# Performance work log

Measured on AMD Instinct MI355X. Metric: run time of the kernel, lower is better.

Reference implementation:

```python
import jax, jax.numpy as jnp
import numpy as np

N_NODES = 50000
N_EDGES = 800000
N_GRAPHS = 128
D_IN, D_HID, D_OUT = 128, 128, 128  # gnn_input_dim, gnn_hidden_dim, gnn_output_dim
EPS = 1e-5
NEG_SLOPE = 0.01


def setup_inputs() -> dict:
    key = jax.random.key(0)
    ks = jax.random.split(key, 16)
    x = jax.random.normal(ks[0], (N_NODES, D_IN), jnp.float32)
    edge_index = jax.random.randint(ks[1], (2, N_EDGES), 0, N_NODES, dtype=jnp.int64)
    batch = jnp.sort(jax.random.randint(ks[2], (N_NODES,), 0, N_GRAPHS, dtype=jnp.int64))

    def lin(k, fi, fo):
        return jax.random.normal(k, (fi, fo), jnp.float32) * (1.0 / np.sqrt(fi))

    d2, d4 = 2 * D_HID, 4 * D_HID
    return {
        "x": x, "edge_index": edge_index, "batch": batch, "batch_size": N_GRAPHS,
        "W1": lin(ks[3], D_IN, d2), "b1": jnp.zeros((d2,), jnp.float32),
        "g1": jnp.ones((d2,), jnp.float32), "be1": jnp.zeros((d2,), jnp.float32),
        "W2": lin(ks[4], d2, d4), "b2": jnp.zeros((d4,), jnp.float32),
        "g2": jnp.ones((d4,), jnp.float32), "be2": jnp.zeros((d4,), jnp.float32),
        "W3": lin(ks[5], d4, d4), "b3": jnp.zeros((d4,), jnp.float32),
        "g3": jnp.ones((d4,), jnp.float32), "be3": jnp.zeros((d4,), jnp.float32),
        "Wf": lin(ks[6], d4, D_OUT), "bf": jnp.zeros((D_OUT,), jnp.float32),
    }


def _layernorm(h, g, b):
    mu = jnp.mean(h, axis=-1, keepdims=True)
    var = jnp.mean(jnp.square(h - mu), axis=-1, keepdims=True)
    return (h - mu) * jax.lax.rsqrt(var + EPS) * g + b


def _gcn_conv(h, W, b, src, dst, norm, n):
    # h' = D^-1/2 (A+I) D^-1/2 (h W) + b   (PyG GCNConv with self-loops)
    m = h @ W                                    # [N, F_out]
    msg = m[src] * norm[:, None]                 # [E+N, F_out]
    return jax.ops.segment_sum(msg, dst, num_segments=n) + b


def reference(x, edge_index, batch, batch_size, W1, b1, g1, be1,
              W2, b2, g2, be2, W3, b3, g3, be3, Wf, bf):
    n = x.shape[0]
    loop = jnp.arange(n, dtype=edge_index.dtype)
    src = jnp.concatenate([edge_index[0], loop])
    dst = jnp.concatenate([edge_index[1], loop])
    deg = jax.ops.segment_sum(jnp.ones_like(dst, dtype=x.dtype), dst, num_segments=n)
    dinv = jax.lax.rsqrt(deg)                    # deg >= 1 due to self loops
    norm = dinv[src] * dinv[dst]

    h = _gcn_conv(x, W1, b1, src, dst, norm, n)
    h = jax.nn.leaky_relu(_layernorm(h, g1, be1), NEG_SLOPE)
    h = _gcn_conv(h, W2, b2, src, dst, norm, n)
    h = jax.nn.leaky_relu(_layernorm(h, g2, be2), NEG_SLOPE)
    h = _gcn_conv(h, W3, b3, src, dst, norm, n)
    h = _layernorm(h, g3, be3)

    # global average pool per graph
    sums = jax.ops.segment_sum(h, batch, num_segments=batch_size)
    cnt = jax.ops.segment_sum(jnp.ones((n,), h.dtype), batch, num_segments=batch_size)
    pooled = sums / jnp.maximum(cnt, 1.0)[:, None]
    return pooled @ Wf + bf
```

## Files before the change

kernel.cpp:

```cpp
#include <hip/hip_runtime.h>
#include <hip/hip_bf16.h>
#include <math.h>

#define GRAPHS 128
#define SCAN_B 256
#define BM 128
#define BN 128
#define PCH 128
#define WSCALE 2097152.0f

typedef __attribute__((ext_vector_type(4))) int i32x4;

__device__ inline unsigned short f2b(float f) {
    unsigned int u = __float_as_uint(f);
    unsigned int r = (u + 0x7fffu + ((u >> 16) & 1u)) >> 16;
    return (unsigned short)r;
}
__device__ inline float b2f(unsigned short u) {
    return __uint_as_float(((unsigned int)u) << 16);
}
__device__ inline void unpack8(float* v, uint4 u) {
    v[0] = b2f(u.x & 0xffffu); v[1] = b2f(u.x >> 16);
    v[2] = b2f(u.y & 0xffffu); v[3] = b2f(u.y >> 16);
    v[4] = b2f(u.z & 0xffffu); v[5] = b2f(u.z >> 16);
    v[6] = b2f(u.w & 0xffffu); v[7] = b2f(u.w >> 16);
}

__device__ inline void gload16(const void* g, void* l) {
    typedef unsigned int __attribute__((address_space(1))) gu32;
    typedef unsigned int __attribute__((address_space(3))) su32;
    __builtin_amdgcn_global_load_lds((const gu32*)g, (su32*)l, 16, 0, 0);
}

__device__ inline int xcd_vid(int p, int nwg) {
    int q = nwg >> 3, r = nwg & 7, x = p & 7, ix = p >> 3;
    return (x < r ? x * (q + 1) : r * (q + 1) + (x - r) * q) + ix;
}


__global__ void k_count(const int* __restrict__ dst, int* __restrict__ cnt, int E) {
    int i = blockIdx.x * blockDim.x + threadIdx.x;
    if (i < E) atomicAdd(&cnt[dst[i]], 1);
}

__global__ void k_scan1(const int* __restrict__ cnt, int* __restrict__ excl,
                        int* __restrict__ bsum, int n) {
    __shared__ int sh[SCAN_B];
    int t = threadIdx.x;
    int i = blockIdx.x * SCAN_B + t;
    int v = (i < n) ? cnt[i] : 0;
    sh[t] = v;
    __syncthreads();
    for (int off = 1; off < SCAN_B; off <<= 1) {
        int x = (t >= off) ? sh[t - off] : 0;
        __syncthreads();
        sh[t] += x;
        __syncthreads();
    }
    if (i < n) excl[i] = sh[t] - v;
    if (t == SCAN_B - 1) bsum[blockIdx.x] = sh[t];
}

__global__ void k_scan2(int* __restrict__ bsum, int nb) {
    __shared__ int sh[SCAN_B];
    int t = threadIdx.x;
    int v = (t < nb) ? bsum[t] : 0;
    sh[t] = v;
    __syncthreads();
    for (int off = 1; off < SCAN_B; off <<= 1) {
        int x = (t >= off) ? sh[t - off] : 0;
        __syncthreads();
        sh[t] += x;
        __syncthreads();
    }
    if (t < nb) bsum[t] = sh[t] - v;
}

__global__ void k_scan3(int* __restrict__ rowstart, const int* __restrict__ bsum,
                        const int* __restrict__ cnt, float* __restrict__ dinv,
                        int* __restrict__ cursor, int n, int E) {
    int i = blockIdx.x * SCAN_B + threadIdx.x;
    if (i < n) {
        rowstart[i] += bsum[blockIdx.x];
        cursor[i] = 0;
        dinv[i] = rsqrtf((float)cnt[i] + 1.0f);
    }
    if (i == 0) rowstart[n] = E;
}

__global__ void k_scatter_csr(const int* __restrict__ src, const int* __restrict__ dst,
                              const float* __restrict__ dinv, const int* __restrict__ rowstart,
                              int* __restrict__ cursor, int2* __restrict__ csr, int E) {
    int e = blockIdx.x * blockDim.x + threadIdx.x;
    if (e >= E) return;
    int s = src[e], d = dst[e];
    int pos = rowstart[d] + atomicAdd(&cursor[d], 1);
    int2 c;
    c.x = s;
    c.y = __float_as_int(dinv[s] * dinv[d]);
    csr[pos] = c;
}


__global__ void k_prep(const float* __restrict__ W1, const float* __restrict__ W2,
                       const float* __restrict__ W3, signed char* __restrict__ T1,
                       signed char* __restrict__ T2, signed char* __restrict__ T3,
                       float* __restrict__ S1, float* __restrict__ S2,
                       float* __restrict__ S3, const float* __restrict__ x,
                       signed char* __restrict__ qx, float* __restrict__ sx,
                       int n, int mpad) {
    int lane = threadIdx.x & 63;
    if (blockIdx.x < 320) {
        int w = blockIdx.x * 4 + (threadIdx.x >> 6);
        const float* W; signed char* T; float* S; int K, N, col;
        if (w < 256) { W = W1; T = T1; S = S1; K = 128; N = 256; col = w; }
        else if (w < 768) { W = W2; T = T2; S = S2; K = 256; N = 512; col = w - 256; }
        else { W = W3; T = T3; S = S3; K = 512; N = 512; col = w - 768; }
        int epl = K >> 6;
        float v[8];
        float mx = 0.f;
        for (int j = 0; j < epl; ++j) {
            float xx = W[(size_t)(lane * epl + j) * N + col];
            v[j] = xx;
            mx = fmaxf(mx, fabsf(xx));
        }
#pragma unroll
        for (int m = 1; m < 64; m <<= 1) mx = fmaxf(mx, __shfl_xor(mx, m));
        float inv = (mx > 0.f) ? 127.0f / mx : 0.f;
        signed char* tp = T + (size_t)col * K + lane * epl;
        for (int j = 0; j < epl; ++j) tp[j] = (signed char)__float2int_rn(v[j] * inv);
        if (lane == 0) S[col] = mx * (1.0f / 127.0f);
        return;
    }
    int row = (blockIdx.x - 320) * 4 + (threadIdx.x >> 6);
    if (row >= mpad) return;
    signed char* qp = qx + (size_t)row * 128 + lane * 2;
    if (row >= n) {
        *(unsigned short*)qp = 0;
        if (lane == 0) sx[row] = 0.f;
        return;
    }
    float2 v = *(const float2*)(x + (size_t)row * 128 + lane * 2);
    float mx = fmaxf(fabsf(v.x), fabsf(v.y));
#pragma unroll
    for (int m = 1; m < 64; m <<= 1) mx = fmaxf(mx, __shfl_xor(mx, m));
    float inv = (mx > 0.f) ? 127.0f / mx : 0.f;
    int q0 = __float2int_rn(v.x * inv), q1 = __float2int_rn(v.y * inv);
    *(unsigned short*)qp = (unsigned short)((q0 & 0xff) | ((q1 & 0xff) << 8));
    if (lane == 0) sx[row] = mx * (1.0f / 127.0f);
}


__device__ inline void accw(int* a, unsigned int u, int wq) {
    a[0] += __mul24((int)(signed char)(u), wq);
    a[1] += __mul24((int)(signed char)(u >> 8), wq);
    a[2] += __mul24((int)(signed char)(u >> 16), wq);
    a[3] += __mul24((int)(signed char)(u >> 24), wq);
}
__device__ inline void acc16(int* a, uint4 u, int wq) {
    accw(a, u.x, wq);
    accw(a + 4, u.y, wq);
    accw(a + 8, u.z, wq);
    accw(a + 12, u.w, wq);
}

template <int F>
__global__ void k_agg8(const signed char* __restrict__ q8, const float* __restrict__ scale,
                       signed char* __restrict__ qa, float* __restrict__ sa,
                       const int* __restrict__ rowstart, const int2* __restrict__ csr,
                       const float* __restrict__ dinv, int n, int mpad) {
    constexpr int TPN = F / 16;
    constexpr int NPB = 256 / TPN;
    int node = blockIdx.x * NPB + (int)(threadIdx.x / TPN);
    int sub = (int)(threadIdx.x % TPN);
    int fo = sub * 16;
    if (node >= mpad) return;
    signed char* outp = qa + (size_t)node * F + fo;
    if (node >= n) {
        uint4 z = {0u, 0u, 0u, 0u};
        *(uint4*)outp = z;
        if (sub == 0) sa[node] = 0.f;
        return;
    }

    const signed char* qf = q8 + fo;
    float di = dinv[node];
    int a[16] = {};
    {
        uint4 u = *(const uint4*)(qf + (size_t)node * F);
        int wq = __float2int_rn(di * di * scale[node] * WSCALE);
        acc16(a, u, wq);
    }
    int b = rowstart[node], e = rowstart[node + 1];
    int j = b;
    for (; j + 2 <= e; j += 2) {
        int2 c0 = csr[j], c1 = csr[j + 1];
        uint4 u0 = *(const uint4*)(qf + (size_t)c0.x * F);
        uint4 u1 = *(const uint4*)(qf + (size_t)c1.x * F);
        int w0 = __float2int_rn(__int_as_float(c0.y) * scale[c0.x] * WSCALE);
        int w1 = __float2int_rn(__int_as_float(c1.y) * scale[c1.x] * WSCALE);
        acc16(a, u0, w0);
        acc16(a, u1, w1);
    }
    for (; j < e; ++j) {
        int2 c = csr[j];
        uint4 u = *(const uint4*)(qf + (size_t)c.x * F);
        int wq = __float2int_rn(__int_as_float(c.y) * scale[c.x] * WSCALE);
        acc16(a, u, wq);
    }
    int amax = 0;
#pragma unroll
    for (int k = 0; k < 16; ++k) amax = max(amax, abs(a[k]));
#pragma unroll
    for (int m = 1; m < TPN; m <<= 1) amax = max(amax, __shfl_xor(amax, m));

    float inv = (amax > 0) ? 127.0f / (float)amax : 0.f;
    unsigned int ob[4];
#pragma unroll
    for (int wi = 0; wi < 4; ++wi) {
        unsigned int o = 0;
#pragma unroll
        for (int k = 0; k < 4; ++k)
            o |= ((unsigned)(__float2int_rn((float)a[wi * 4 + k] * inv) & 0xff)) << (8 * k);
        ob[wi] = o;
    }
    *(uint4*)outp = *(uint4*)ob;
    if (sub == 0) sa[node] = (float)amax * (1.0f / (127.0f * WSCALE));
}


__global__ __launch_bounds__(256) void k_gemm_i8(
    const signed char* __restrict__ A, const float* __restrict__ srow,
    const signed char* __restrict__ BT, const float* __restrict__ scol,
    const float* __restrict__ bias, unsigned short* __restrict__ C,
    int K, int N, int ncb) {
    __shared__ __align__(16) char sA[BM * 128];
    __shared__ __align__(16) char sB[BN * 128];

    const int vid = xcd_vid((int)blockIdx.x, (int)gridDim.x);
    const int rb = vid / ncb;
    const int cb = vid - rb * ncb;
    const int tid = threadIdx.x;
    const int lane = tid & 63;
    const int wave = tid >> 6;
    const int wr = wave >> 1, wc = wave & 1;
    const size_t row0 = (size_t)rb * BM;
    const size_t col0 = (size_t)cb * BN;

    const signed char* srcA[4];
    const signed char* srcB[4];
    char* dstA[4];
    char* dstB[4];
#pragma unroll
    for (int c = 0; c < 4; ++c) {
        int idx = c * 256 + tid;
        int row = idx >> 3;
        int cbl = ((idx & 7) << 4) ^ ((row & 7) << 4);
        srcA[c] = A + (row0 + row) * K + cbl;
        srcB[c] = BT + (col0 + row) * K + cbl;
        dstA[c] = sA + idx * 16;
        dstB[c] = sB + idx * 16;
    }

    const int fr = lane & 15;
    const int fg = lane >> 4;
    const int fsw = (lane & 7) << 4;
    int offA[4][2], offB[4][2];
#pragma unroll
    for (int t = 0; t < 4; ++t)
#pragma unroll
        for (int kk = 0; kk < 2; ++kk) {
            offA[t][kk] = (wr * 64 + t * 16 + fr) * 128 + ((kk * 64 + fg * 16) ^ fsw);
            offB[t][kk] = (wc * 64 + t * 16 + fr) * 128 + ((kk * 64 + fg * 16) ^ fsw);
        }

    i32x4 acc[4][4] = {};

    for (int k0 = 0; k0 < K; k0 += 128) {
#pragma unroll
        for (int c = 0; c < 4; ++c) gload16(srcA[c] + k0, dstA[c]);
#pragma unroll
        for (int c = 0; c < 4; ++c) gload16(srcB[c] + k0, dstB[c]);
        __syncthreads();
#pragma unroll
        for (int kk = 0; kk < 2; ++kk) {
            i32x4 av[4], bv[4];
#pragma unroll
            for (int t = 0; t < 4; ++t) av[t] = *(const i32x4*)(sA + offA[t][kk]);
#pragma unroll
            for (int t = 0; t < 4; ++t) bv[t] = *(const i32x4*)(sB + offB[t][kk]);
#pragma unroll
            for (int i = 0; i < 4; ++i)
#pragma unroll
                for (int j = 0; j < 4; ++j)
                    acc[i][j] = __builtin_amdgcn_mfma_i32_16x16x64_i8(av[i], bv[j],
                                                                      acc[i][j], 0, 0, 0);
        }
        __syncthreads();
    }

    float sr[4][4];
#pragma unroll
    for (int i = 0; i < 4; ++i)
#pragma unroll
        for (int q = 0; q < 4; ++q)
            sr[i][q] = srow[row0 + wr * 64 + i * 16 + fg * 4 + q];

#pragma unroll
    for (int i = 0; i < 4; ++i) {
#pragma unroll
        for (int j = 0; j < 4; ++j) {
            size_t r = row0 + wr * 64 + i * 16 + fg * 4;
            size_t cc = col0 + wc * 64 + j * 16 + fr;
            float scc = scol[cc];
            float bb = bias[cc];
#pragma unroll
            for (int q = 0; q < 4; ++q)
                C[(r + q) * N + cc] = f2b((float)acc[i][j][q] * (sr[i][q] * scc) + bb);
        }
    }
}


template <int F, bool LRELU>
__global__ void k_lnr8(const unsigned short* __restrict__ z, signed char* __restrict__ q8,
                       float* __restrict__ scale, const float* __restrict__ g,
                       const float* __restrict__ be, int mpad) {
    constexpr int V = F / 64;
    int row = blockIdx.x * 4 + (threadIdx.x >> 6);
    int lane = threadIdx.x & 63;
    const unsigned short* p = z + (size_t)row * F + lane * V;
    float v[V];
    if constexpr (V == 8) {
        uint4 u = *(const uint4*)p;
        unpack8(v, u);
    } else {
        uint2 u = *(const uint2*)p;
        v[0] = b2f(u.x & 0xffffu); v[1] = b2f(u.x >> 16);
        v[2] = b2f(u.y & 0xffffu); v[3] = b2f(u.y >> 16);
    }
    float s = 0.f, q = 0.f;
#pragma unroll
    for (int k = 0; k < V; ++k) { s += v[k]; q += v[k] * v[k]; }
#pragma unroll
    for (int m = 1; m < 64; m <<= 1) {
        s += __shfl_xor(s, m);
        q += __shfl_xor(q, m);
    }
    float mu = s * (1.0f / F);
    float var = q * (1.0f / F) - mu * mu;
    float rs = rsqrtf(var + 1e-5f);

    float y[V];
    float mx = 0.f;
#pragma unroll
    for (int k = 0; k < V; ++k) {
        float yy = (v[k] - mu) * rs * g[lane * V + k] + be[lane * V + k];
        if (LRELU) yy = fmaxf(yy, 0.f) + 0.01f * fminf(yy, 0.f);
        y[k] = yy;
        mx = fmaxf(mx, fabsf(yy));
    }
#pragma unroll
    for (int m = 1; m < 64; m <<= 1) mx = fmaxf(mx, __shfl_xor(mx, m));

    float inv = (mx > 0.f) ? 127.0f / mx : 0.f;
    unsigned int ob[V / 4];
#pragma unroll
    for (int k = 0; k < V; k += 4) {
        int q0 = __float2int_rn(y[k] * inv);
        int q1 = __float2int_rn(y[k + 1] * inv);
        int q2 = __float2int_rn(y[k + 2] * inv);
        int q3 = __float2int_rn(y[k + 3] * inv);
        ob[k / 4] = (q0 & 0xff) | ((q1 & 0xff) << 8) | ((q2 & 0xff) << 16) | ((q3 & 0xff) << 24);
    }
    signed char* qp = q8 + (size_t)row * F + lane * V;
    if constexpr (V == 8) *(uint2*)qp = *(uint2*)ob;
    else                  *(unsigned int*)qp = ob[0];
    if (lane == 0) scale[row] = mx * (1.0f / 127.0f);
}


__global__ void k_pool4(const unsigned short* __restrict__ z, const float* __restrict__ g,
                        const float* __restrict__ be, const int* __restrict__ batch,
                        float* __restrict__ pooled, int n) {
    int i0 = blockIdx.x * PCH;
    int iend = i0 + PCH; if (iend > n) iend = n;
    int w = threadIdx.x >> 6, lane = threadIdx.x & 63;
    int f0 = lane * 8;
    float gk[8], ek[8];
    {
        float4 ga = *(const float4*)(g + f0), gb = *(const float4*)(g + f0 + 4);
        float4 ea = *(const float4*)(be + f0), eb = *(const float4*)(be + f0 + 4);
        gk[0] = ga.x; gk[1] = ga.y; gk[2] = ga.z; gk[3] = ga.w;
        gk[4] = gb.x; gk[5] = gb.y; gk[6] = gb.z; gk[7] = gb.w;
        ek[0] = ea.x; ek[1] = ea.y; ek[2] = ea.z; ek[3] = ea.w;
        ek[4] = eb.x; ek[5] = eb.y; ek[6] = eb.z; ek[7] = eb.w;
    }
    float a[8] = {};
    int cur = -1;
    for (int i = i0 + w; i < iend; i += 4) {
        int gg = batch[i];
        if (gg != cur) {
            if (cur >= 0) {
                float* pp = pooled + (size_t)cur * 512 + f0;
#pragma unroll
                for (int k = 0; k < 8; ++k) atomicAdd(&pp[k], a[k]);
            }
#pragma unroll
            for (int k = 0; k < 8; ++k) a[k] = 0.f;
            cur = gg;
        }
        uint4 u = *(const uint4*)(z + (size_t)i * 512 + f0);
        float v[8]; unpack8(v, u);
        float s = 0.f, q = 0.f;
#pragma unroll
        for (int k = 0; k < 8; ++k) { s += v[k]; q += v[k] * v[k]; }
#pragma unroll
        for (int m = 1; m < 64; m <<= 1) {
            s += __shfl_xor(s, m);
            q += __shfl_xor(q, m);
        }
        float mu = s * (1.0f / 512.0f);
        float var = q * (1.0f / 512.0f) - mu * mu;
        float rs = rsqrtf(var + 1e-5f);
#pragma unroll
        for (int k = 0; k < 8; ++k) a[k] += (v[k] - mu) * rs * gk[k] + ek[k];
    }
    if (cur >= 0) {
        float* pp = pooled + (size_t)cur * 512 + f0;
#pragma unroll
        for (int k = 0; k < 8; ++k) atomicAdd(&pp[k], a[k]);
    }
}


__global__ void k_final(const float* __restrict__ pooled, const int* __restrict__ batch,
                        const float* __restrict__ Wf, const float* __restrict__ bf,
                        float* __restrict__ out, int n) {
    int gph = blockIdx.x;
    int o = threadIdx.x;
    int lo = 0, hi = n;
    while (lo < hi) { int mid = (lo + hi) >> 1; if (batch[mid] < gph) lo = mid + 1; else hi = mid; }
    int start = lo;
    lo = start; hi = n;
    while (lo < hi) { int mid = (lo + hi) >> 1; if (batch[mid] < gph + 1) lo = mid + 1; else hi = mid; }
    int end = lo;
    float inv = 1.0f / fmaxf((float)(end - start), 1.0f);

    __shared__ float p[512];
    for (int k = threadIdx.x; k < 512; k += 128) p[k] = pooled[(size_t)gph * 512 + k] * inv;
    __syncthreads();
    float acc = bf[o];
#pragma unroll 8
    for (int k = 0; k < 512; ++k) acc += p[k] * Wf[(size_t)k * 128 + o];
    out[(size_t)gph * 128 + o] = acc;
}


static inline size_t align_up(size_t x) { return (x + 255) & ~(size_t)255; }

extern "C" void kernel_launch(void* const* d_in, const int* in_sizes, int n_in,
                              void* d_out, int out_size, void* d_ws, size_t ws_size,
                              hipStream_t stream) {
    const float* x     = (const float*)d_in[0];
    const int*   ei    = (const int*)d_in[1];
    const int*   batch = (const int*)d_in[2];
    const float* W1 = (const float*)d_in[4],  *b1 = (const float*)d_in[5];
    const float* g1 = (const float*)d_in[6],  *be1= (const float*)d_in[7];
    const float* W2 = (const float*)d_in[8],  *b2 = (const float*)d_in[9];
    const float* g2 = (const float*)d_in[10], *be2= (const float*)d_in[11];
    const float* W3 = (const float*)d_in[12], *b3 = (const float*)d_in[13];
    const float* g3 = (const float*)d_in[14], *be3= (const float*)d_in[15];
    const float* Wf = (const float*)d_in[16], *bf = (const float*)d_in[17];
    float* out = (float*)d_out;

    const int N = in_sizes[0] / 128;
    const int E = in_sizes[1] / 2;
    const int Mpad = ((N + BM - 1) / BM) * BM;
    const int* src = ei;
    const int* dst = ei + E;

    char* ws = (char*)d_ws;
    size_t off = 0;
    auto take = [&](size_t bytes) { char* p = ws + off; off += align_up(bytes); return p; };

    unsigned short* zb      = (unsigned short*)take((size_t)Mpad * 512 * 2);
    signed char*    qa      = (signed char*)take((size_t)Mpad * 512);
    float*          sa      = (float*)take((size_t)Mpad * 4);
    signed char*    q8      = (signed char*)take((size_t)Mpad * 512);
    float*          scale   = (float*)take((size_t)Mpad * 4);
    signed char*    q8x     = (signed char*)take((size_t)Mpad * 128);
    float*          sx      = (float*)take((size_t)Mpad * 4);
    signed char*    wq1     = (signed char*)take((size_t)256 * 128);
    signed char*    wq2     = (signed char*)take((size_t)512 * 256);
    signed char*    wq3     = (signed char*)take((size_t)512 * 512);
    float*          sc1     = (float*)take(256 * 4);
    float*          sc2     = (float*)take(512 * 4);
    float*          sc3     = (float*)take(512 * 4);
    float*          dinv    = (float*)take((size_t)N * 4);
    int*            rowstart= (int*)  take((size_t)(N + 1) * 4);
    int*            cnt     = (int*)  take((size_t)N * 4);
    int*            cursor  = (int*)  take((size_t)N * 4);
    int*            bsum    = (int*)  take((size_t)SCAN_B * 4);
    int2*           csr     = (int2*) take((size_t)E * 8);
    float*          pooled  = (float*)take((size_t)GRAPHS * 512 * 4);

    const int nb = (N + SCAN_B - 1) / SCAN_B;
    const int NR4 = Mpad / 4;

    hipMemsetAsync(cnt, 0, (size_t)N * 4, stream);
    k_count<<<(E + 255) / 256, 256, 0, stream>>>(dst, cnt, E);
    k_scan1<<<nb, SCAN_B, 0, stream>>>(cnt, rowstart, bsum, N);
    k_scan2<<<1, SCAN_B, 0, stream>>>(bsum, nb);
    k_scan3<<<nb, SCAN_B, 0, stream>>>(rowstart, bsum, cnt, dinv, cursor, N, E);
    k_scatter_csr<<<(E + 255) / 256, 256, 0, stream>>>(src, dst, dinv, rowstart, cursor, csr, E);

    k_prep<<<320 + NR4, 256, 0, stream>>>(W1, W2, W3, wq1, wq2, wq3, sc1, sc2, sc3,
                                          x, q8x, sx, N, Mpad);

    k_agg8<128><<<Mpad / 32, 256, 0, stream>>>(q8x, sx, qa, sa, rowstart, csr, dinv, N, Mpad);
    k_gemm_i8<<<(Mpad / BM) * 2, 256, 0, stream>>>(qa, sa, wq1, sc1, b1, zb, 128, 256, 2);
    k_lnr8<256, true><<<NR4, 256, 0, stream>>>(zb, q8, scale, g1, be1, Mpad);

    k_agg8<256><<<Mpad / 16, 256, 0, stream>>>(q8, scale, qa, sa, rowstart, csr, dinv, N, Mpad);
    k_gemm_i8<<<(Mpad / BM) * 4, 256, 0, stream>>>(qa, sa, wq2, sc2, b2, zb, 256, 512, 4);
    k_lnr8<512, true><<<NR4, 256, 0, stream>>>(zb, q8, scale, g2, be2, Mpad);

    k_agg8<512><<<Mpad / 8, 256, 0, stream>>>(q8, scale, qa, sa, rowstart, csr, dinv, N, Mpad);
    k_gemm_i8<<<(Mpad / BM) * 4, 256, 0, stream>>>(qa, sa, wq3, sc3, b3, zb, 512, 512, 4);

    hipMemsetAsync(pooled, 0, (size_t)GRAPHS * 512 * 4, stream);
    k_pool4<<<(N + PCH - 1) / PCH, 256, 0, stream>>>(zb, g3, be3, batch, pooled, N);
    k_final<<<GRAPHS, 128, 0, stream>>>(pooled, batch, Wf, bf, out, N);
}
```

Baseline: 394.1 us.

## Use fixed per-layer int8 quantization scale from LayerNorm affine bounds

Replaces the per-row dynamic int8 scale after LayerNorm with a per-layer constant scale derived from the max |gamma| and |beta|, computed in an extra block of the prep kernel. Aggregation then no longer gathers a per-neighbor scale for each edge, and LayerNorm skips its max reduction and scale store. The two workspace memsets are merged into one by placing the buffers next to each other. The fixed bound assumes normalized values stay within about six standard deviations; larger values are clamped, which risks accuracy loss.

```diff
diff --git a/kernel.cpp b/kernel.cpp
--- a/kernel.cpp
+++ b/kernel.cpp
@@ -108,8 +108,35 @@
                        float* __restrict__ S1, float* __restrict__ S2,
                        float* __restrict__ S3, const float* __restrict__ x,
                        signed char* __restrict__ qx, float* __restrict__ sx,
-                       int n, int mpad) {
+                       const float* __restrict__ g1, const float* __restrict__ be1,
+                       const float* __restrict__ g2, const float* __restrict__ be2,
+                       float* __restrict__ scf, float* __restrict__ scfi,
+                       int n, int mpad, int nblk) {
     int lane = threadIdx.x & 63;
+    if ((int)blockIdx.x == nblk - 1) {
+        int w = threadIdx.x >> 6;
+        if (w < 2) {
+            const float* g = w ? g2 : g1;
+            const float* be = w ? be2 : be1;
+            int nn = w ? 512 : 256;
+            float mg = 0.f, mb = 0.f;
+            for (int i = lane; i < nn; i += 64) {
+                mg = fmaxf(mg, fabsf(g[i]));
+                mb = fmaxf(mb, fabsf(be[i]));
+            }
+#pragma unroll
+            for (int m = 1; m < 64; m <<= 1) {
+                mg = fmaxf(mg, __shfl_xor(mg, m));
+                mb = fmaxf(mb, __shfl_xor(mb, m));
+            }
+            if (lane == 0) {
+                float s = (6.0f * mg + mb) * (1.0f / 127.0f);
+                scf[w] = s;
+                scfi[w] = 1.0f / s;
+            }
+        }
+        return;
+    }
     if (blockIdx.x < 320) {
         int w = blockIdx.x * 4 + (threadIdx.x >> 6);
         const float* W; signed char* T; float* S; int K, N, col;
@@ -164,8 +191,9 @@
     accw(a + 12, u.w, wq);
 }
 
-template <int F>
+template <int F, bool FIXS>
 __global__ void k_agg8(const signed char* __restrict__ q8, const float* __restrict__ scale,
+                       const float* __restrict__ scf, int li,
                        signed char* __restrict__ qa, float* __restrict__ sa,
                        const int* __restrict__ rowstart, const int2* __restrict__ csr,
                        const float* __restrict__ dinv, int n, int mpad) {
@@ -183,13 +211,14 @@
         return;
     }
 
+    float kconst = FIXS ? scf[li] * WSCALE : 0.f;
     const signed char* qf = q8 + fo;
     float di = dinv[node];
     int a[16] = {};
     {
         uint4 u = *(const uint4*)(qf + (size_t)node * F);
-        int wq = __float2int_rn(di * di * scale[node] * WSCALE);
-        acc16(a, u, wq);
+        float ws = FIXS ? di * di * kconst : di * di * scale[node] * WSCALE;
+        acc16(a, u, __float2int_rn(ws));
     }
     int b = rowstart[node], e = rowstart[node + 1];
     int j = b;
@@ -197,15 +226,22 @@
         int2 c0 = csr[j], c1 = csr[j + 1];
         uint4 u0 = *(const uint4*)(qf + (size_t)c0.x * F);
         uint4 u1 = *(const uint4*)(qf + (size_t)c1.x * F);
-        int w0 = __float2int_rn(__int_as_float(c0.y) * scale[c0.x] * WSCALE);
-        int w1 = __float2int_rn(__int_as_float(c1.y) * scale[c1.x] * WSCALE);
+        int w0, w1;
+        if (FIXS) {
+            w0 = __float2int_rn(__int_as_float(c0.y) * kconst);
+            w1 = __float2int_rn(__int_as_float(c1.y) * kconst);
+        } else {
+            w0 = __float2int_rn(__int_as_float(c0.y) * scale[c0.x] * WSCALE);
+            w1 = __float2int_rn(__int_as_float(c1.y) * scale[c1.x] * WSCALE);
+        }
         acc16(a, u0, w0);
         acc16(a, u1, w1);
     }
     for (; j < e; ++j) {
         int2 c = csr[j];
         uint4 u = *(const uint4*)(qf + (size_t)c.x * F);
-        int wq = __float2int_rn(__int_as_float(c.y) * scale[c.x] * WSCALE);
+        int wq = FIXS ? __float2int_rn(__int_as_float(c.y) * kconst)
+                      : __float2int_rn(__int_as_float(c.y) * scale[c.x] * WSCALE);
         acc16(a, u, wq);
     }
     int amax = 0;
@@ -323,9 +359,9 @@
 
 
 template <int F, bool LRELU>
-__global__ void k_lnr8(const unsigned short* __restrict__ z, signed char* __restrict__ q8,
-                       float* __restrict__ scale, const float* __restrict__ g,
-                       const float* __restrict__ be, int mpad) {
+__global__ void k_lnq(const unsigned short* __restrict__ z, signed char* __restrict__ q8,
+                      const float* __restrict__ scfi, int li,
+                      const float* __restrict__ g, const float* __restrict__ be, int mpad) {
     constexpr int V = F / 64;
     int row = blockIdx.x * 4 + (threadIdx.x >> 6);
     int lane = threadIdx.x & 63;
@@ -350,33 +386,25 @@
     float mu = s * (1.0f / F);
     float var = q * (1.0f / F) - mu * mu;
     float rs = rsqrtf(var + 1e-5f);
-
-    float y[V];
-    float mx = 0.f;
-#pragma unroll
-    for (int k = 0; k < V; ++k) {
-        float yy = (v[k] - mu) * rs * g[lane * V + k] + be[lane * V + k];
-        if (LRELU) yy = fmaxf(yy, 0.f) + 0.01f * fminf(yy, 0.f);
-        y[k] = yy;
-        mx = fmaxf(mx, fabsf(yy));
-    }
-#pragma unroll
-    for (int m = 1; m < 64; m <<= 1) mx = fmaxf(mx, __shfl_xor(mx, m));
-
-    float inv = (mx > 0.f) ? 127.0f / mx : 0.f;
+    float inv = scfi[li];
+
     unsigned int ob[V / 4];
 #pragma unroll
     for (int k = 0; k < V; k += 4) {
-        int q0 = __float2int_rn(y[k] * inv);
-        int q1 = __float2int_rn(y[k + 1] * inv);
-        int q2 = __float2int_rn(y[k + 2] * inv);
-        int q3 = __float2int_rn(y[k + 3] * inv);
-        ob[k / 4] = (q0 & 0xff) | ((q1 & 0xff) << 8) | ((q2 & 0xff) << 16) | ((q3 & 0xff) << 24);
+        unsigned int o = 0;
+#pragma unroll
+        for (int t = 0; t < 4; ++t) {
+            float yy = (v[k + t] - mu) * rs * g[lane * V + k + t] + be[lane * V + k + t];
+            if (LRELU) yy = fmaxf(yy, 0.f) + 0.01f * fminf(yy, 0.f);
+            int qi = __float2int_rn(yy * inv);
+            qi = min(127, max(-127, qi));
+            o |= ((unsigned)(qi & 0xff)) << (8 * t);
+        }
+        ob[k / 4] = o;
     }
     signed char* qp = q8 + (size_t)row * F + lane * V;
     if constexpr (V == 8) *(uint2*)qp = *(uint2*)ob;
     else                  *(unsigned int*)qp = ob[0];
-    if (lane == 0) scale[row] = mx * (1.0f / 127.0f);
 }
 
 
@@ -484,11 +512,12 @@
     size_t off = 0;
     auto take = [&](size_t bytes) { char* p = ws + off; off += align_up(bytes); return p; };
 
+    int*            cnt     = (int*)  take((size_t)N * 4);
+    float*          pooled  = (float*)take((size_t)GRAPHS * 512 * 4);
     unsigned short* zb      = (unsigned short*)take((size_t)Mpad * 512 * 2);
     signed char*    qa      = (signed char*)take((size_t)Mpad * 512);
     float*          sa      = (float*)take((size_t)Mpad * 4);
     signed char*    q8      = (signed char*)take((size_t)Mpad * 512);
-    float*          scale   = (float*)take((size_t)Mpad * 4);
     signed char*    q8x     = (signed char*)take((size_t)Mpad * 128);
     float*          sx      = (float*)take((size_t)Mpad * 4);
     signed char*    wq1     = (signed char*)take((size_t)256 * 128);
@@ -497,39 +526,43 @@
     float*          sc1     = (float*)take(256 * 4);
     float*          sc2     = (float*)take(512 * 4);
     float*          sc3     = (float*)take(512 * 4);
+    float*          scf     = (float*)take(2 * 4);
+    float*          scfi    = (float*)take(2 * 4);
     float*          dinv    = (float*)take((size_t)N * 4);
     int*            rowstart= (int*)  take((size_t)(N + 1) * 4);
-    int*            cnt     = (int*)  take((size_t)N * 4);
     int*            cursor  = (int*)  take((size_t)N * 4);
     int*            bsum    = (int*)  take((size_t)SCAN_B * 4);
     int2*           csr     = (int2*) take((size_t)E * 8);
-    float*          pooled  = (float*)take((size_t)GRAPHS * 512 * 4);
 
     const int nb = (N + SCAN_B - 1) / SCAN_B;
     const int NR4 = Mpad / 4;
-
-    hipMemsetAsync(cnt, 0, (size_t)N * 4, stream);
+    const int nprep = 320 + NR4 + 1;
+
+    hipMemsetAsync(cnt, 0, (size_t)((char*)(pooled + GRAPHS * 512) - (char*)cnt), stream);
+
     k_count<<<(E + 255) / 256, 256, 0, stream>>>(dst, cnt, E);
     k_scan1<<<nb, SCAN_B, 0, stream>>>(cnt, rowstart, bsum, N);
     k_scan2<<<1, SCAN_B, 0, stream>>>(bsum, nb);
     k_scan3<<<nb, SCAN_B, 0, stream>>>(rowstart, bsum, cnt, dinv, cursor, N, E);
     k_scatter_csr<<<(E + 255) / 256, 256, 0, stream>>>(src, dst, dinv, rowstart, cursor, csr, E);
 
-    k_prep<<<320 + NR4, 256, 0, stream>>>(W1, W2, W3, wq1, wq2, wq3, sc1, sc2, sc3,
-                                          x, q8x, sx, N, Mpad);
-
-    k_agg8<128><<<Mpad / 32, 256, 0, stream>>>(q8x, sx, qa, sa, rowstart, csr, dinv, N, Mpad);
+    k_prep<<<nprep, 256, 0, stream>>>(W1, W2, W3, wq1, wq2, wq3, sc1, sc2, sc3,
+                                      x, q8x, sx, g1, be1, g2, be2, scf, scfi, N, Mpad, nprep);
+
+    k_agg8<128, false><<<Mpad / 32, 256, 0, stream>>>(q8x, sx, nullptr, 0, qa, sa,
+                                                      rowstart, csr, dinv, N, Mpad);
     k_gemm_i8<<<(Mpad / BM) * 2, 256, 0, stream>>>(qa, sa, wq1, sc1, b1, zb, 128, 256, 2);
-    k_lnr8<256, true><<<NR4, 256, 0, stream>>>(zb, q8, scale, g1, be1, Mpad);
-
-    k_agg8<256><<<Mpad / 16, 256, 0, stream>>>(q8, scale, qa, sa, rowstart, csr, dinv, N, Mpad);
+    k_lnq<256, true><<<NR4, 256, 0, stream>>>(zb, q8, scfi, 0, g1, be1, Mpad);
+
+    k_agg8<256, true><<<Mpad / 16, 256, 0, stream>>>(q8, nullptr, scf, 0, qa, sa,
+                                                     rowstart, csr, dinv, N, Mpad);
     k_gemm_i8<<<(Mpad / BM) * 4, 256, 0, stream>>>(qa, sa, wq2, sc2, b2, zb, 256, 512, 4);
-    k_lnr8<512, true><<<NR4, 256, 0, stream>>>(zb, q8, scale, g2, be2, Mpad);
-
-    k_agg8<512><<<Mpad / 8, 256, 0, stream>>>(q8, scale, qa, sa, rowstart, csr, dinv, N, Mpad);
+    k_lnq<512, true><<<NR4, 256, 0, stream>>>(zb, q8, scfi, 1, g2, be2, Mpad);
+
+    k_agg8<512, true><<<Mpad / 8, 256, 0, stream>>>(q8, nullptr, scf, 1, qa, sa,
+                                                    rowstart, csr, dinv, N, Mpad);
     k_gemm_i8<<<(Mpad / BM) * 4, 256, 0, stream>>>(qa, sa, wq3, sc3, b3, zb, 512, 512, 4);
 
-    hipMemsetAsync(pooled, 0, (size_t)GRAPHS * 512 * 4, stream);
     k_pool4<<<(N + PCH - 1) / PCH, 256, 0, stream>>>(zb, g3, be3, batch, pooled, N);
     k_final<<<GRAPHS, 128, 0, stream>>>(pooled, batch, Wf, bf, out, N);
 }
```

After: 389.0 us. Within noise of the previous version (-1.3%).
